# Kernel tuning notes

Hardware: AMD Instinct MI355X
Metric: run time of the kernel (lower is better)

## Reference

```python
import jax, jax.numpy as jnp
import numpy as np
from jax import lax

GROUPS = 32


def _fps(xyz, m):
    # farthest point sampling; indices are non-differentiable selections
    xyz = lax.stop_gradient(xyz)
    B, N, _ = xyz.shape

    def step(carry, _):
        dist, far = carry
        c = jnp.take_along_axis(xyz, far[:, None, None], axis=1)  # [B,1,3]
        d = jnp.sum((xyz - c) ** 2, axis=-1)                       # [B,N]
        dist = jnp.minimum(dist, d)
        return (dist, jnp.argmax(dist, axis=1)), far

    init = (jnp.full((B, N), 1e10, xyz.dtype), jnp.zeros((B,), jnp.int32))
    _, cent = lax.scan(step, init, None, length=m)
    return jnp.transpose(cent)  # [B,m]


def _sqdist(a, b):
    # [B,Na,3] x [B,Nb,3] -> [B,Na,Nb]
    return (jnp.sum(a * a, -1)[:, :, None] + jnp.sum(b * b, -1)[:, None, :]
            - 2.0 * jnp.einsum('bnc,bmc->bnm', a, b))


def _gather(feat, idx):
    # feat [B,S,C], idx [B,N,k] -> [B,N,k,C]
    return jax.vmap(lambda f, i: f[i])(feat, idx)


def _edge_conv(f, idx, W, b):
    nbr = _gather(f, idx)                                # [B,S,k,C]
    ctr = jnp.broadcast_to(f[:, :, None, :], nbr.shape)
    e = jnp.concatenate([ctr, nbr - ctr], axis=-1)       # [B,S,k,2C]
    h = jax.nn.relu(jnp.einsum('bske,ec->bskc', e, W) + b)
    return jnp.max(h, axis=2)                            # [B,S,C']


def _graph_encoder(x, k, layers, Wo, bo):
    d2 = _sqdist(x[..., :3], x[..., :3])
    idx = lax.top_k(-d2, k)[1]                           # kNN on coords (incl. self)
    f = x
    for W, b in layers:
        f = _edge_conv(f, idx, W, b)
    return f @ Wo + bo


def _upsample(fs, xd, xs):
    # 3-NN inverse-distance interpolation, matches torch.cdist/topk path
    d = jnp.sqrt(jnp.maximum(_sqdist(xd, xs), 0.0))      # euclidean like cdist
    negv, idx = lax.top_k(-d, 3)
    w = 1.0 / (-negv + 1e-8)
    w = w / jnp.sum(w, -1, keepdims=True)
    fk = _gather(fs, idx)                                # [B,Nd,3,C]
    return jnp.sum(fk * w[..., None], axis=2)


def _group_norm(x, g, b):
    B, N, C = x.shape
    xg = x.reshape(B, N, GROUPS, C // GROUPS)
    mu = xg.mean(-1, keepdims=True)
    var = xg.var(-1, keepdims=True)
    xn = ((xg - mu) * lax.rsqrt(var + 1e-5)).reshape(B, N, C)
    return xn * g + b


def _pos_encoding(N, d):
    pos = jnp.arange(N, dtype=jnp.float32)[:, None]
    div = jnp.exp(jnp.arange(0, d, 2, dtype=jnp.float32) * (-np.log(10000.0) / d))
    ang = pos * div
    return jnp.stack([jnp.sin(ang), jnp.cos(ang)], axis=-1).reshape(N, d)


def _forward(x,
             e1_W0, e1_b0, e1_W1, e1_b1, e1_Wo, e1_bo,
             e2_W0, e2_b0, e2_W1, e2_b1, e2_Wo, e2_bo,
             e3_W0, e3_b0, e3_W1, e3_b1, e3_W2, e3_b2, e3_Wo, e3_bo,
             f_W1, f_b1, g1_w, g1_b, f_W2, f_b2, g2_w, g2_b):
    B, N, C = x.shape
    encs = [
        (512, 16, [(e1_W0, e1_b0), (e1_W1, e1_b1)], e1_Wo, e1_bo),
        (1024, 32, [(e2_W0, e2_b0), (e2_W1, e2_b1)], e2_Wo, e2_bo),
        (2048, 64, [(e3_W0, e3_b0), (e3_W1, e3_b1), (e3_W2, e3_b2)], e3_Wo, e3_bo),
    ]
    feats = []
    for scale, k, layers, Wo, bo in encs:
        if N > scale:
            idx = _fps(x[..., :3], scale)
            xs = jnp.take_along_axis(x, idx[:, :, None], axis=1)  # [B,scale,C]
        else:
            xs = x
        f = _graph_encoder(xs, k, layers, Wo, bo)
        if f.shape[1] < N:
            f = _upsample(f, x[..., :3], xs[..., :3])
        feats.append(f)
    fused = jnp.concatenate(feats, axis=-1)               # [B,N,1280]
    h = jax.nn.relu(_group_norm(fused @ f_W1 + f_b1, g1_w, g1_b))
    h = jax.nn.relu(_group_norm(h @ f_W2 + f_b2, g2_w, g2_b))
    return h + _pos_encoding(N, h.shape[-1])[None]


def setup_inputs() -> dict:
    key = jax.random.key(0)
    ks = iter(jax.random.split(key, 64))

    def W(shape, s=0.05):
        return jax.random.normal(next(ks), shape, jnp.float32) * s

    inp = {"x": jax.random.normal(next(ks), (2, 4096, 6), jnp.float32)}
    # encoder 1: in 6, hidden [128,256], out 256, k=16
    inp.update(e1_W0=W((12, 128)), e1_b0=jnp.zeros(128), e1_W1=W((256, 256)), e1_b1=jnp.zeros(256),
               e1_Wo=W((256, 256)), e1_bo=jnp.zeros(256))
    # encoder 2: in 6, hidden [256,512], out 512, k=32
    inp.update(e2_W0=W((12, 256)), e2_b0=jnp.zeros(256), e2_W1=W((512, 512)), e2_b1=jnp.zeros(512),
               e2_Wo=W((512, 512)), e2_bo=jnp.zeros(512))
    # encoder 3: in 6, hidden [128,256,512], out 512, k=64
    inp.update(e3_W0=W((12, 128)), e3_b0=jnp.zeros(128), e3_W1=W((256, 256)), e3_b1=jnp.zeros(256),
               e3_W2=W((512, 512)), e3_b2=jnp.zeros(512), e3_Wo=W((512, 512)), e3_bo=jnp.zeros(512))
    # fusion: 1280 -> 512 -> 512 with GroupNorm(32, 512)
    inp.update(f_W1=W((1280, 512)), f_b1=jnp.zeros(512), g1_w=jnp.ones(512), g1_b=jnp.zeros(512),
               f_W2=W((512, 512)), f_b2=jnp.zeros(512), g2_w=jnp.ones(512), g2_b=jnp.zeros(512))
    return inp


def reference(x,
              e1_W0, e1_b0, e1_W1, e1_b1, e1_Wo, e1_bo,
              e2_W0, e2_b0, e2_W1, e2_b1, e2_Wo, e2_bo,
              e3_W0, e3_b0, e3_W1, e3_b1, e3_W2, e3_b2, e3_Wo, e3_bo,
              f_W1, f_b1, g1_w, g1_b, f_W2, f_b2, g2_w, g2_b):
    return _forward(x,
                    e1_W0, e1_b0, e1_W1, e1_b1, e1_Wo, e1_bo,
                    e2_W0, e2_b0, e2_W1, e2_b1, e2_Wo, e2_bo,
                    e3_W0, e3_b0, e3_W1, e3_b1, e3_W2, e3_b2, e3_Wo, e3_bo,
                    f_W1, f_b1, g1_w, g1_b, f_W2, f_b2, g2_w, g2_b)
```

## Files before the change

kernel.cpp:

```cpp
#include <hip/hip_runtime.h>
#include <math.h>

#define OFF_CENT   0x0
#define OFF_XSP    0x20000
#define OFF_XS6    0x40000
#define OFF_KNN    0x60000
#define OFF_F      0x180000
#define OFF_UV     0xA00000
#define OFF_G      0x1A00000
#define OFF_WCAT   0x2200000
#define OFF_BCAT   0x2400000
#define OFF_FUSED  0x2500000
#define OFF_T      0x180000
#define OFF_H1     0x1200000
#define OFF_T2     0x2200000

__device__ __forceinline__ unsigned fkey_flip(float f) {
  unsigned u = __float_as_uint(f);
  return u ^ ((u >> 31) ? 0xFFFFFFFFu : 0x80000000u);
}
__device__ __forceinline__ float fkey_unflip(unsigned k) {
  unsigned u = k ^ ((k >> 31) ? 0x80000000u : 0xFFFFFFFFu);
  return __uint_as_float(u);
}

template<int CTRL>
__device__ __forceinline__ float dpp_max_stepf(float v) {
  int t = __builtin_amdgcn_update_dpp(__float_as_int(v), __float_as_int(v),
                                      CTRL, 0xf, 0xf, false);
  return fmaxf(v, __int_as_float(t));
}
__device__ __forceinline__ float wave64_max(float v) {
  v = dpp_max_stepf<0x111>(v);
  v = dpp_max_stepf<0x112>(v);
  v = dpp_max_stepf<0x114>(v);
  v = dpp_max_stepf<0x118>(v);
  v = dpp_max_stepf<0x142>(v);
  v = dpp_max_stepf<0x143>(v);
  return __int_as_float(__builtin_amdgcn_readlane(__float_as_int(v), 63));
}
__device__ __forceinline__ unsigned long long u64max(unsigned long long a,
                                                    unsigned long long b) {
  return a > b ? a : b;
}

__global__ __launch_bounds__(512) void fps_kernel(const float* __restrict__ x,
                                                  int* __restrict__ cent)
{
  int b = blockIdx.x, tid = threadIdx.x;
  __shared__ float4 C4[4096];
  __shared__ __align__(16) unsigned long long slots[2][8];
  float px[8], py[8], pz[8], dist[8];
#pragma unroll
  for (int i = 0; i < 8; ++i) {
    int p = tid + 512 * i;
    const float* r = x + ((long)b * 4096 + p) * 6;
    px[i] = r[0]; py[i] = r[1]; pz[i] = r[2];
    C4[p] = make_float4(px[i], py[i], pz[i], 0.0f);
    dist[i] = 1e10f;
  }
  if (tid == 0) cent[b * 2048] = 0;
  __syncthreads();
  float4 c0 = C4[0];
  float cx = c0.x, cy = c0.y, cz = c0.z;
  int wid = tid >> 6, lane = tid & 63;
  for (int j = 1; j < 2048; ++j) {
    float m = -1.0f;
#pragma unroll
    for (int i = 0; i < 8; ++i) {
      float dx = __fsub_rn(px[i], cx);
      float dy = __fsub_rn(py[i], cy);
      float dz = __fsub_rn(pz[i], cz);
      float d  = __fadd_rn(__fadd_rn(__fmul_rn(dx,dx), __fmul_rn(dy,dy)), __fmul_rn(dz,dz));
      float nd = fminf(dist[i], d);
      dist[i] = nd;
      m = fmaxf(m, nd);
    }
    float wm = wave64_max(m);
    unsigned long long mm = 0ULL; unsigned ii = 0;
#pragma unroll
    for (int i = 7; i >= 0; --i) {
      unsigned long long mi = __ballot(dist[i] == wm);
      if (mi) { mm = mi; ii = (unsigned)i; }
    }
    int lane_w = __ffsll((unsigned long long)mm) - 1;
    unsigned idx_w = (unsigned)(wid * 64 + lane_w) + 512u * ii;
    if (lane == 0)
      slots[j & 1][wid] = ((unsigned long long)__float_as_uint(wm) << 32)
                        | (unsigned)(0xFFFFFFFFu - idx_w);
    __syncthreads();
    const unsigned long long* sl = slots[j & 1];
    ulonglong2 sA = *(const ulonglong2*)&sl[0];
    ulonglong2 sB = *(const ulonglong2*)&sl[2];
    ulonglong2 sC = *(const ulonglong2*)&sl[4];
    ulonglong2 sD = *(const ulonglong2*)&sl[6];
    unsigned long long kk = u64max(u64max(u64max(sA.x, sA.y), u64max(sB.x, sB.y)),
                                   u64max(u64max(sC.x, sC.y), u64max(sD.x, sD.y)));
    unsigned idx = 0xFFFFFFFFu - (unsigned)kk;
    float4 c = C4[idx];
    cx = c.x; cy = c.y; cz = c.z;
    if (tid == 0) cent[b * 2048 + j] = idx;
  }
}

__global__ void gather_xs_kernel(const float* __restrict__ x, const int* __restrict__ cent,
                                 float* __restrict__ xs6, float4* __restrict__ xsp)
{
  int t = blockIdx.x * 256 + threadIdx.x;
  if (t >= 2 * 2048) return;
  int b = t >> 11;
  int p = cent[t];
  const float* src = x + ((long)b * 4096 + p) * 6;
  float* dst = xs6 + (long)t * 6;
#pragma unroll
  for (int c = 0; c < 6; ++c) dst[c] = src[c];
  xsp[t] = make_float4(src[0], src[1], src[2], 0.0f);
}

template<int S, int K>
__global__ __launch_bounds__(256) void knn_kernel(const float4* __restrict__ xsp,
                                                  int* __restrict__ out)
{
  constexpr int NI = S / 64;
  __shared__ float4 P[S];
  int b = (blockIdx.x * 4) / S;
  int wid = threadIdx.x >> 6, lane = threadIdx.x & 63;
  int s = (blockIdx.x * 4 + wid) & (S - 1);
  for (int i = threadIdx.x; i < S; i += 256) P[i] = xsp[b * 2048 + i];
  __syncthreads();
  float4 Q = P[s];
  float saq = __fadd_rn(__fadd_rn(__fmul_rn(Q.x,Q.x), __fmul_rn(Q.y,Q.y)), __fmul_rn(Q.z,Q.z));
  float dd[NI];
#pragma unroll
  for (int i = 0; i < NI; ++i) {
    float4 c = P[i * 64 + lane];
    float sac = __fadd_rn(__fadd_rn(__fmul_rn(c.x,c.x), __fmul_rn(c.y,c.y)), __fmul_rn(c.z,c.z));
    float dot = __fadd_rn(__fadd_rn(__fmul_rn(Q.x,c.x), __fmul_rn(Q.y,c.y)), __fmul_rn(Q.z,c.z));
    dd[i] = __fsub_rn(__fadd_rn(saq, sac), __fmul_rn(2.0f, dot));
  }
  long obase = ((long)b * S + s) * K;
  for (int t = 0; t < K; ++t) {
    float bv = INFINITY; int bi = 0;
#pragma unroll
    for (int i = 0; i < NI; ++i) if (dd[i] < bv) { bv = dd[i]; bi = i; }
    unsigned long long key = ((unsigned long long)fkey_flip(bv) << 32)
                           | (unsigned)(bi * 64 + lane);
#pragma unroll
    for (int m = 32; m; m >>= 1) {
      unsigned long long o = __shfl_xor(key, m, 64);
      if (o < key) key = o;
    }
    unsigned cand = (unsigned)key;
    if ((int)(cand & 63) == lane) {
      int slot = cand >> 6;
#pragma unroll
      for (int i = 0; i < NI; ++i) if (i == slot) dd[i] = INFINITY;
    }
    if (lane == 0) out[obase + t] = (int)cand;
  }
}

__global__ void wcat_prep(const float* __restrict__ W, const float* __restrict__ bias,
                          int C, int Cp, float* __restrict__ Wcat, float* __restrict__ bcat)
{
  int n2 = 2 * Cp;
  int total = C * n2;
  for (int t = blockIdx.x * 256 + threadIdx.x; t < total + n2; t += gridDim.x * 256) {
    if (t < total) {
      int c = t / n2, n = t % n2;
      Wcat[t] = (n < Cp) ? (W[c * Cp + n] - W[(C + c) * Cp + n]) : W[(C + c) * Cp + (n - Cp)];
    } else {
      int n = t - total;
      bcat[n] = (n < Cp) ? bias[n] : 0.0f;
    }
  }
}

__global__ __launch_bounds__(256) void gemm_bias(
    const float* __restrict__ A, long strideA, int lda,
    const float* __restrict__ W, int N, int K,
    const float* __restrict__ bias,
    float* __restrict__ C, long strideC, int ldc)
{
  A += (long)blockIdx.z * strideA;
  C += (long)blockIdx.z * strideC;
  int rowBase = blockIdx.x * 64, colBase = blockIdx.y * 64;
  __shared__ float As[16][68];
  __shared__ float Ws[16][68];
  int tid = threadIdx.x;
  int tx = tid & 15, ty = tid >> 4;
  float acc[4][4] = {};
  for (int k0 = 0; k0 < K; k0 += 16) {
    {
      int r = tid >> 2, c0 = (tid & 3) * 4;
      const float* Ar = A + (long)(rowBase + r) * lda + k0 + c0;
#pragma unroll
      for (int u = 0; u < 4; ++u) {
        float val = 0.0f;
        if (k0 + c0 + u < K) val = Ar[u];
        As[c0 + u][r] = val;
      }
    }
    {
      int c = tid & 63, kr = tid >> 6;
#pragma unroll
      for (int u = 0; u < 4; ++u) {
        int kk = kr + u * 4;
        float val = 0.0f;
        if (k0 + kk < K) val = W[(long)(k0 + kk) * N + colBase + c];
        Ws[kk][c] = val;
      }
    }
    __syncthreads();
#pragma unroll
    for (int kk = 0; kk < 16; ++kk) {
      float4 av = *(const float4*)&As[kk][ty * 4];
      float4 wv = *(const float4*)&Ws[kk][tx * 4];
      float a_[4] = {av.x, av.y, av.z, av.w};
      float w_[4] = {wv.x, wv.y, wv.z, wv.w};
#pragma unroll
      for (int i = 0; i < 4; ++i)
#pragma unroll
        for (int j = 0; j < 4; ++j)
          acc[i][j] = fmaf(a_[i], w_[j], acc[i][j]);
    }
    __syncthreads();
  }
#pragma unroll
  for (int i = 0; i < 4; ++i) {
    int r = rowBase + ty * 4 + i;
    int c0 = colBase + tx * 4;
    float4 o;
    o.x = acc[i][0] + bias[c0 + 0];
    o.y = acc[i][1] + bias[c0 + 1];
    o.z = acc[i][2] + bias[c0 + 2];
    o.w = acc[i][3] + bias[c0 + 3];
    *(float4*)&C[(long)r * ldc + c0] = o;
  }
}

__global__ __launch_bounds__(256) void gemm_bias_big(
    const float* __restrict__ A, int lda,
    const float* __restrict__ W, int N, int K,
    const float* __restrict__ bias,
    float* __restrict__ C, int ldc)
{
  int rowBase = blockIdx.x * 128, colBase = blockIdx.y * 128;
  __shared__ float As[16][132];
  __shared__ float Ws[16][132];
  int tid = threadIdx.x;
  int tx = tid & 15, ty = tid >> 4;
  float acc[8][8] = {};
  for (int k0 = 0; k0 < K; k0 += 16) {
    {
      int r = tid >> 1, c0 = (tid & 1) * 8;
      const float* Ar = A + (long)(rowBase + r) * lda + k0 + c0;
      float4 v0 = *(const float4*)(Ar);
      float4 v1 = *(const float4*)(Ar + 4);
      As[c0 + 0][r] = v0.x; As[c0 + 1][r] = v0.y; As[c0 + 2][r] = v0.z; As[c0 + 3][r] = v0.w;
      As[c0 + 4][r] = v1.x; As[c0 + 5][r] = v1.y; As[c0 + 6][r] = v1.z; As[c0 + 7][r] = v1.w;
    }
    {
      int kr = tid >> 4, c0 = (tid & 15) * 8;
      const float* Wr = W + (long)(k0 + kr) * N + colBase + c0;
      float4 w0 = *(const float4*)(Wr);
      float4 w1 = *(const float4*)(Wr + 4);
      *(float4*)&Ws[kr][c0]     = w0;
      *(float4*)&Ws[kr][c0 + 4] = w1;
    }
    __syncthreads();
#pragma unroll
    for (int kk = 0; kk < 16; ++kk) {
      float a_[8], w_[8];
      *(float4*)&a_[0] = *(const float4*)&As[kk][ty * 8];
      *(float4*)&a_[4] = *(const float4*)&As[kk][ty * 8 + 4];
      *(float4*)&w_[0] = *(const float4*)&Ws[kk][tx * 8];
      *(float4*)&w_[4] = *(const float4*)&Ws[kk][tx * 8 + 4];
#pragma unroll
      for (int i = 0; i < 8; ++i)
#pragma unroll
        for (int jj = 0; jj < 8; ++jj)
          acc[i][jj] = fmaf(a_[i], w_[jj], acc[i][jj]);
    }
    __syncthreads();
  }
#pragma unroll
  for (int i = 0; i < 8; ++i) {
    int r = rowBase + ty * 8 + i;
    int c0 = colBase + tx * 8;
    float4 o0, o1;
    o0.x = acc[i][0] + bias[c0 + 0];
    o0.y = acc[i][1] + bias[c0 + 1];
    o0.z = acc[i][2] + bias[c0 + 2];
    o0.w = acc[i][3] + bias[c0 + 3];
    o1.x = acc[i][4] + bias[c0 + 4];
    o1.y = acc[i][5] + bias[c0 + 5];
    o1.z = acc[i][6] + bias[c0 + 6];
    o1.w = acc[i][7] + bias[c0 + 7];
    *(float4*)&C[(long)r * ldc + c0]     = o0;
    *(float4*)&C[(long)r * ldc + c0 + 4] = o1;
  }
}

__global__ void edge_agg(const float* __restrict__ UV, const int* __restrict__ idx,
                         int S, int k, int Cp, float* __restrict__ F)
{
  int bs = blockIdx.x;
  int b = bs / S;
  __shared__ int nb[64];
  if ((int)threadIdx.x < k) nb[threadIdx.x] = idx[(long)bs * k + threadIdx.x];
  __syncthreads();
  int ld = 2 * Cp;
  const float* Ub = UV + (long)bs * ld;
  for (int c = threadIdx.x; c < Cp; c += blockDim.x) {
    float m = -INFINITY;
    for (int j = 0; j < k; ++j) {
      float v = UV[(long)(b * S + nb[j]) * ld + Cp + c];
      m = fmaxf(m, v);
    }
    float r = Ub[c] + m;
    F[(long)bs * Cp + c] = r > 0.0f ? r : 0.0f;
  }
}

template<int S, int CP>
__global__ __launch_bounds__(256) void upsample_kernel(
    const float* __restrict__ x, const float4* __restrict__ xsp,
    const float* __restrict__ G, float* __restrict__ fused, int colOff)
{
  constexpr int NI = S / 64;
  __shared__ float4 P[S];
  int b = (blockIdx.x * 4) >> 12;
  int wid = threadIdx.x >> 6, lane = threadIdx.x & 63;
  int n = (blockIdx.x * 4 + wid) & 4095;
  for (int i = threadIdx.x; i < S; i += 256) P[i] = xsp[b * 2048 + i];
  __syncthreads();
  const float* q = x + ((long)b * 4096 + n) * 6;
  float qx = q[0], qy = q[1], qz = q[2];
  float saq = __fadd_rn(__fadd_rn(__fmul_rn(qx,qx), __fmul_rn(qy,qy)), __fmul_rn(qz,qz));
  float dd[NI];
#pragma unroll
  for (int i = 0; i < NI; ++i) {
    float4 c = P[i * 64 + lane];
    float sac = __fadd_rn(__fadd_rn(__fmul_rn(c.x,c.x), __fmul_rn(c.y,c.y)), __fmul_rn(c.z,c.z));
    float dot = __fadd_rn(__fadd_rn(__fmul_rn(qx,c.x), __fmul_rn(qy,c.y)), __fmul_rn(qz,c.z));
    dd[i] = __fsub_rn(__fadd_rn(saq, sac), __fmul_rn(2.0f, dot));
  }
  int id[3]; float w[3];
  for (int t = 0; t < 3; ++t) {
    float bv = INFINITY; int bi = 0;
#pragma unroll
    for (int i = 0; i < NI; ++i) if (dd[i] < bv) { bv = dd[i]; bi = i; }
    unsigned long long key = ((unsigned long long)fkey_flip(bv) << 32)
                           | (unsigned)(bi * 64 + lane);
#pragma unroll
    for (int m = 32; m; m >>= 1) {
      unsigned long long o = __shfl_xor(key, m, 64);
      if (o < key) key = o;
    }
    unsigned cand = (unsigned)key;
    float d2 = fkey_unflip((unsigned)(key >> 32));
    float d = __fsqrt_rn(fmaxf(d2, 0.0f));
    id[t] = (int)cand;
    w[t] = 1.0f / __fadd_rn(d, 1e-8f);
    if ((int)(cand & 63) == lane) {
      int slot = cand >> 6;
#pragma unroll
      for (int i = 0; i < NI; ++i) if (i == slot) dd[i] = INFINITY;
    }
  }
  float wsum = __fadd_rn(__fadd_rn(w[0], w[1]), w[2]);
  float w0 = w[0] / wsum, w1 = w[1] / wsum, w2 = w[2] / wsum;
  const float* g0 = G + (long)(b * S + id[0]) * CP;
  const float* g1 = G + (long)(b * S + id[1]) * CP;
  const float* g2 = G + (long)(b * S + id[2]) * CP;
  float* orow = fused + ((long)b * 4096 + n) * 1280 + colOff;
#pragma unroll
  for (int t = 0; t < CP / 64; ++t) {
    int c = lane + 64 * t;
    float v = __fadd_rn(__fadd_rn(__fmul_rn(w0, g0[c]), __fmul_rn(w1, g1[c])),
                        __fmul_rn(w2, g2[c]));
    orow[c] = v;
  }
}

__global__ __launch_bounds__(256) void gn_kernel(const float* __restrict__ T,
    const float* __restrict__ gw, const float* __restrict__ gb,
    float* __restrict__ out, int addPos)
{
  int t = blockIdx.x * 256 + threadIdx.x;
  int row = t >> 5, g = t & 31;
  const float* p = T + (long)row * 512 + g * 16;
  float v[16];
#pragma unroll
  for (int i = 0; i < 4; ++i) {
    float4 f = *(const float4*)(p + i * 4);
    v[i*4+0] = f.x; v[i*4+1] = f.y; v[i*4+2] = f.z; v[i*4+3] = f.w;
  }
  float s = 0.0f;
#pragma unroll
  for (int i = 0; i < 16; ++i) s += v[i];
  float mu = s * 0.0625f;
  float var = 0.0f;
#pragma unroll
  for (int i = 0; i < 16; ++i) { float d = v[i] - mu; var += d * d; }
  var *= 0.0625f;
  float inv = 1.0f / sqrtf(var + 1e-5f);
  int cbase = g * 16;
  int n = row & 4095;
  float o[16];
#pragma unroll
  for (int i = 0; i < 16; ++i) {
    int c = cbase + i;
    float y = (v[i] - mu) * inv * gw[c] + gb[c];
    y = y > 0.0f ? y : 0.0f;
    if (addPos) {
      int half = c >> 1;
      float div = expf((float)(2 * half) * -0.017988946039016358f);
      float ang = (float)n * div;
      y += (c & 1) ? cosf(ang) : sinf(ang);
    }
    o[i] = y;
  }
  float* d = out + (long)row * 512 + cbase;
#pragma unroll
  for (int i = 0; i < 4; ++i) {
    float4 f; f.x = o[i*4+0]; f.y = o[i*4+1]; f.z = o[i*4+2]; f.w = o[i*4+3];
    *(float4*)(d + i * 4) = f;
  }
}

static inline void launch_gemm(const float* A, long strideA, int lda,
                               const float* W, const float* bias,
                               float* C, long strideC, int ldc,
                               int Mb, int N, int K, int nb, hipStream_t s)
{
  dim3 grid(Mb / 64, N / 64, nb);
  gemm_bias<<<grid, 256, 0, s>>>(A, strideA, lda, W, N, K, bias, C, strideC, ldc);
}
static inline void launch_gemm_big(const float* A, int lda,
                                   const float* W, const float* bias,
                                   float* C, int ldc,
                                   int M, int N, int K, hipStream_t s)
{
  dim3 grid(M / 128, N / 128, 1);
  gemm_bias_big<<<grid, 256, 0, s>>>(A, lda, W, N, K, bias, C, ldc);
}

extern "C" void kernel_launch(void* const* d_in, const int* in_sizes, int n_in,
                              void* d_out, int out_size, void* d_ws, size_t ws_size,
                              hipStream_t stream)
{
  const float* x     = (const float*)d_in[0];
  const float* e1_W0 = (const float*)d_in[1];  const float* e1_b0 = (const float*)d_in[2];
  const float* e1_W1 = (const float*)d_in[3];  const float* e1_b1 = (const float*)d_in[4];
  const float* e1_Wo = (const float*)d_in[5];  const float* e1_bo = (const float*)d_in[6];
  const float* e2_W0 = (const float*)d_in[7];  const float* e2_b0 = (const float*)d_in[8];
  const float* e2_W1 = (const float*)d_in[9];  const float* e2_b1 = (const float*)d_in[10];
  const float* e2_Wo = (const float*)d_in[11]; const float* e2_bo = (const float*)d_in[12];
  const float* e3_W0 = (const float*)d_in[13]; const float* e3_b0 = (const float*)d_in[14];
  const float* e3_W1 = (const float*)d_in[15]; const float* e3_b1 = (const float*)d_in[16];
  const float* e3_W2 = (const float*)d_in[17]; const float* e3_b2 = (const float*)d_in[18];
  const float* e3_Wo = (const float*)d_in[19]; const float* e3_bo = (const float*)d_in[20];
  const float* f_W1  = (const float*)d_in[21]; const float* f_b1  = (const float*)d_in[22];
  const float* g1_w  = (const float*)d_in[23]; const float* g1_b  = (const float*)d_in[24];
  const float* f_W2  = (const float*)d_in[25]; const float* f_b2  = (const float*)d_in[26];
  const float* g2_w  = (const float*)d_in[27]; const float* g2_b  = (const float*)d_in[28];

  char* ws = (char*)d_ws;
  int*    cent  = (int*)(ws + OFF_CENT);
  float4* xsp   = (float4*)(ws + OFF_XSP);
  float*  xs6   = (float*)(ws + OFF_XS6);
  int*    knn   = (int*)(ws + OFF_KNN);
  float*  F     = (float*)(ws + OFF_F);
  float*  UV    = (float*)(ws + OFF_UV);
  float*  G     = (float*)(ws + OFF_G);
  float*  WCAT  = (float*)(ws + OFF_WCAT);
  float*  BCAT  = (float*)(ws + OFF_BCAT);
  float*  FUSED = (float*)(ws + OFF_FUSED);
  float*  T     = (float*)(ws + OFF_T);
  float*  H1    = (float*)(ws + OFF_H1);
  float*  T2    = (float*)(ws + OFF_T2);

  fps_kernel<<<2, 512, 0, stream>>>(x, cent);
  gather_xs_kernel<<<16, 256, 0, stream>>>(x, cent, xs6, xsp);

  knn_kernel<512,16><<<256, 256, 0, stream>>>(xsp, knn);
  wcat_prep<<<256, 256, 0, stream>>>(e1_W0, e1_b0, 6, 128, WCAT, BCAT);
  launch_gemm(xs6, (long)2048*6, 6, WCAT, BCAT, UV, (long)512*256, 256, 512, 256, 6, 2, stream);
  edge_agg<<<dim3(2*512), 128, 0, stream>>>(UV, knn, 512, 16, 128, F);
  wcat_prep<<<256, 256, 0, stream>>>(e1_W1, e1_b1, 128, 256, WCAT, BCAT);
  launch_gemm(F, 0, 128, WCAT, BCAT, UV, 0, 512, 1024, 512, 128, 1, stream);
  edge_agg<<<dim3(2*512), 256, 0, stream>>>(UV, knn, 512, 16, 256, F);
  launch_gemm(F, 0, 256, e1_Wo, e1_bo, G, 0, 256, 1024, 256, 256, 1, stream);
  upsample_kernel<512,256><<<2048, 256, 0, stream>>>(x, xsp, G, FUSED, 0);

  knn_kernel<1024,32><<<512, 256, 0, stream>>>(xsp, knn);
  wcat_prep<<<256, 256, 0, stream>>>(e2_W0, e2_b0, 6, 256, WCAT, BCAT);
  launch_gemm(xs6, (long)2048*6, 6, WCAT, BCAT, UV, (long)1024*512, 512, 1024, 512, 6, 2, stream);
  edge_agg<<<dim3(2*1024), 256, 0, stream>>>(UV, knn, 1024, 32, 256, F);
  wcat_prep<<<256, 256, 0, stream>>>(e2_W1, e2_b1, 256, 512, WCAT, BCAT);
  launch_gemm_big(F, 256, WCAT, BCAT, UV, 1024, 2048, 1024, 256, stream);
  edge_agg<<<dim3(2*1024), 256, 0, stream>>>(UV, knn, 1024, 32, 512, F);
  launch_gemm(F, 0, 512, e2_Wo, e2_bo, G, 0, 512, 2048, 512, 512, 1, stream);
  upsample_kernel<1024,512><<<2048, 256, 0, stream>>>(x, xsp, G, FUSED, 256);

  knn_kernel<2048,64><<<1024, 256, 0, stream>>>(xsp, knn);
  wcat_prep<<<256, 256, 0, stream>>>(e3_W0, e3_b0, 6, 128, WCAT, BCAT);
  launch_gemm(xs6, (long)2048*6, 6, WCAT, BCAT, UV, (long)2048*256, 256, 2048, 256, 6, 2, stream);
  edge_agg<<<dim3(2*2048), 128, 0, stream>>>(UV, knn, 2048, 64, 128, F);
  wcat_prep<<<256, 256, 0, stream>>>(e3_W1, e3_b1, 128, 256, WCAT, BCAT);
  launch_gemm_big(F, 128, WCAT, BCAT, UV, 512, 4096, 512, 128, stream);
  edge_agg<<<dim3(2*2048), 256, 0, stream>>>(UV, knn, 2048, 64, 256, F);
  wcat_prep<<<256, 256, 0, stream>>>(e3_W2, e3_b2, 256, 512, WCAT, BCAT);
  launch_gemm_big(F, 256, WCAT, BCAT, UV, 1024, 4096, 1024, 256, stream);
  edge_agg<<<dim3(2*2048), 256, 0, stream>>>(UV, knn, 2048, 64, 512, F);
  launch_gemm_big(F, 512, e3_Wo, e3_bo, G, 512, 4096, 512, 512, stream);
  upsample_kernel<2048,512><<<2048, 256, 0, stream>>>(x, xsp, G, FUSED, 768);

  launch_gemm_big(FUSED, 1280, f_W1, f_b1, T, 512, 8192, 512, 1280, stream);
  gn_kernel<<<1024, 256, 0, stream>>>(T, g1_w, g1_b, H1, 0);
  launch_gemm_big(H1, 512, f_W2, f_b2, T2, 512, 8192, 512, 512, stream);
  gn_kernel<<<1024, 256, 0, stream>>>(T2, g2_w, g2_b, (float*)d_out, 1);
}
```

Measured before the change: 2.309 ms.

## Use split-bf16 MFMA GEMM and vectorize edge aggregation and upsample gathers

Replaces the FP32 SIMT 128x128 GEMM with a matrix-core kernel that splits each fp32 operand into high and low bf16 parts and issues three MFMA 16x16x32 products, keeping near-fp32 accuracy. Several medium GEMMs previously on the 64-tile path now use it as well. Edge aggregation and the upsample gather are rewritten to use float4 loads and stores, with the edge thread count tied to channel width. The GEMM loads W with strided scalar reads, writes scalar outputs and has no double buffering, and the bf16x3 scheme loses a little precision compared with fp32.

```diff
diff --git a/kernel.cpp b/kernel.cpp
--- a/kernel.cpp
+++ b/kernel.cpp
@@ -239,67 +239,109 @@
   }
 }
 
-__global__ __launch_bounds__(256) void gemm_bias_big(
+typedef __attribute__((ext_vector_type(8))) short bf16x8;
+typedef __attribute__((ext_vector_type(4))) float f32x4;
+
+__device__ __forceinline__ unsigned short f2bf_rn(float f) {
+  unsigned u = __float_as_uint(f);
+  unsigned r = u + 0x7FFFu + ((u >> 16) & 1u);
+  return (unsigned short)(r >> 16);
+}
+__device__ __forceinline__ float bf2f(unsigned short h) {
+  return __uint_as_float(((unsigned)h) << 16);
+}
+__device__ __forceinline__ void cvt4(const float4 v, int2& hi, int2& lo) {
+  unsigned short h0 = f2bf_rn(v.x), h1 = f2bf_rn(v.y);
+  unsigned short h2 = f2bf_rn(v.z), h3 = f2bf_rn(v.w);
+  unsigned short l0 = f2bf_rn(v.x - bf2f(h0)), l1 = f2bf_rn(v.y - bf2f(h1));
+  unsigned short l2 = f2bf_rn(v.z - bf2f(h2)), l3 = f2bf_rn(v.w - bf2f(h3));
+  hi.x = (int)((unsigned)h0 | ((unsigned)h1 << 16));
+  hi.y = (int)((unsigned)h2 | ((unsigned)h3 << 16));
+  lo.x = (int)((unsigned)l0 | ((unsigned)l1 << 16));
+  lo.y = (int)((unsigned)l2 | ((unsigned)l3 << 16));
+}
+
+__global__ __launch_bounds__(256) void gemm_mfma(
     const float* __restrict__ A, int lda,
     const float* __restrict__ W, int N, int K,
     const float* __restrict__ bias,
     float* __restrict__ C, int ldc)
 {
+  __shared__ unsigned short Ah[128][40], Al[128][40];
+  __shared__ unsigned short Bh[128][40], Bl[128][40];
+  int tid = threadIdx.x;
+  int lane = tid & 63, wv = tid >> 6;
+  int wr = wv >> 1, wc = wv & 1;
+  int l15 = lane & 15, l16 = lane >> 4;
   int rowBase = blockIdx.x * 128, colBase = blockIdx.y * 128;
-  __shared__ float As[16][132];
-  __shared__ float Ws[16][132];
-  int tid = threadIdx.x;
-  int tx = tid & 15, ty = tid >> 4;
-  float acc[8][8] = {};
-  for (int k0 = 0; k0 < K; k0 += 16) {
+  f32x4 acc[4][4];
+#pragma unroll
+  for (int mb = 0; mb < 4; ++mb)
+#pragma unroll
+    for (int nb = 0; nb < 4; ++nb) acc[mb][nb] = 0.0f;
+
+  int r_st = tid >> 1, h_st = tid & 1;
+  for (int k0 = 0; k0 < K; k0 += 32) {
     {
-      int r = tid >> 1, c0 = (tid & 1) * 8;
-      const float* Ar = A + (long)(rowBase + r) * lda + k0 + c0;
-      float4 v0 = *(const float4*)(Ar);
-      float4 v1 = *(const float4*)(Ar + 4);
-      As[c0 + 0][r] = v0.x; As[c0 + 1][r] = v0.y; As[c0 + 2][r] = v0.z; As[c0 + 3][r] = v0.w;
-      As[c0 + 4][r] = v1.x; As[c0 + 5][r] = v1.y; As[c0 + 6][r] = v1.z; As[c0 + 7][r] = v1.w;
+      const float* Ap = A + (long)(rowBase + r_st) * lda + k0 + h_st * 16;
+#pragma unroll
+      for (int e = 0; e < 16; e += 4) {
+        float4 v = *(const float4*)(Ap + e);
+        int2 hi, lo; cvt4(v, hi, lo);
+        *(int2*)&Ah[r_st][h_st * 16 + e] = hi;
+        *(int2*)&Al[r_st][h_st * 16 + e] = lo;
+      }
     }
     {
-      int kr = tid >> 4, c0 = (tid & 15) * 8;
-      const float* Wr = W + (long)(k0 + kr) * N + colBase + c0;
-      float4 w0 = *(const float4*)(Wr);
-      float4 w1 = *(const float4*)(Wr + 4);
-      *(float4*)&Ws[kr][c0]     = w0;
-      *(float4*)&Ws[kr][c0 + 4] = w1;
+      const float* Wp = W + (long)(k0 + h_st * 16) * N + colBase + r_st;
+#pragma unroll
+      for (int e = 0; e < 16; e += 4) {
+        float4 v;
+        v.x = Wp[(long)(e + 0) * N];
+        v.y = Wp[(long)(e + 1) * N];
+        v.z = Wp[(long)(e + 2) * N];
+        v.w = Wp[(long)(e + 3) * N];
+        int2 hi, lo; cvt4(v, hi, lo);
+        *(int2*)&Bh[r_st][h_st * 16 + e] = hi;
+        *(int2*)&Bl[r_st][h_st * 16 + e] = lo;
+      }
     }
     __syncthreads();
-#pragma unroll
-    for (int kk = 0; kk < 16; ++kk) {
-      float a_[8], w_[8];
-      *(float4*)&a_[0] = *(const float4*)&As[kk][ty * 8];
-      *(float4*)&a_[4] = *(const float4*)&As[kk][ty * 8 + 4];
-      *(float4*)&w_[0] = *(const float4*)&Ws[kk][tx * 8];
-      *(float4*)&w_[4] = *(const float4*)&Ws[kk][tx * 8 + 4];
-#pragma unroll
-      for (int i = 0; i < 8; ++i)
-#pragma unroll
-        for (int jj = 0; jj < 8; ++jj)
-          acc[i][jj] = fmaf(a_[i], w_[jj], acc[i][jj]);
-    }
+    bf16x8 ah[4], al[4], bh[4], bl[4];
+#pragma unroll
+    for (int mb = 0; mb < 4; ++mb) {
+      int r = wr * 64 + mb * 16 + l15;
+      ah[mb] = *(const bf16x8*)&Ah[r][l16 * 8];
+      al[mb] = *(const bf16x8*)&Al[r][l16 * 8];
+    }
+#pragma unroll
+    for (int nb = 0; nb < 4; ++nb) {
+      int c = wc * 64 + nb * 16 + l15;
+      bh[nb] = *(const bf16x8*)&Bh[c][l16 * 8];
+      bl[nb] = *(const bf16x8*)&Bl[c][l16 * 8];
+    }
+#pragma unroll
+    for (int mb = 0; mb < 4; ++mb)
+#pragma unroll
+      for (int nb = 0; nb < 4; ++nb) {
+        acc[mb][nb] = __builtin_amdgcn_mfma_f32_16x16x32_bf16(ah[mb], bh[nb], acc[mb][nb], 0, 0, 0);
+        acc[mb][nb] = __builtin_amdgcn_mfma_f32_16x16x32_bf16(al[mb], bh[nb], acc[mb][nb], 0, 0, 0);
+        acc[mb][nb] = __builtin_amdgcn_mfma_f32_16x16x32_bf16(ah[mb], bl[nb], acc[mb][nb], 0, 0, 0);
+      }
     __syncthreads();
   }
 #pragma unroll
-  for (int i = 0; i < 8; ++i) {
-    int r = rowBase + ty * 8 + i;
-    int c0 = colBase + tx * 8;
-    float4 o0, o1;
-    o0.x = acc[i][0] + bias[c0 + 0];
-    o0.y = acc[i][1] + bias[c0 + 1];
-    o0.z = acc[i][2] + bias[c0 + 2];
-    o0.w = acc[i][3] + bias[c0 + 3];
-    o1.x = acc[i][4] + bias[c0 + 4];
-    o1.y = acc[i][5] + bias[c0 + 5];
-    o1.z = acc[i][6] + bias[c0 + 6];
-    o1.w = acc[i][7] + bias[c0 + 7];
-    *(float4*)&C[(long)r * ldc + c0]     = o0;
-    *(float4*)&C[(long)r * ldc + c0 + 4] = o1;
-  }
+  for (int mb = 0; mb < 4; ++mb)
+#pragma unroll
+    for (int nb = 0; nb < 4; ++nb) {
+      int c = colBase + wc * 64 + nb * 16 + l15;
+      float bs = bias[c];
+#pragma unroll
+      for (int r = 0; r < 4; ++r) {
+        int row = rowBase + wr * 64 + mb * 16 + l16 * 4 + r;
+        C[(long)row * ldc + c] = acc[mb][nb][r] + bs;
+      }
+    }
 }
 
 __global__ void edge_agg(const float* __restrict__ UV, const int* __restrict__ idx,
@@ -311,15 +353,23 @@
   if ((int)threadIdx.x < k) nb[threadIdx.x] = idx[(long)bs * k + threadIdx.x];
   __syncthreads();
   int ld = 2 * Cp;
-  const float* Ub = UV + (long)bs * ld;
-  for (int c = threadIdx.x; c < Cp; c += blockDim.x) {
-    float m = -INFINITY;
+  int nf4 = Cp >> 2;
+  for (int c4 = threadIdx.x; c4 < nf4; c4 += blockDim.x) {
+    float4 m = make_float4(-INFINITY, -INFINITY, -INFINITY, -INFINITY);
     for (int j = 0; j < k; ++j) {
-      float v = UV[(long)(b * S + nb[j]) * ld + Cp + c];
-      m = fmaxf(m, v);
-    }
-    float r = Ub[c] + m;
-    F[(long)bs * Cp + c] = r > 0.0f ? r : 0.0f;
+      const float4* vp = (const float4*)(UV + (long)(b * S + nb[j]) * ld + Cp);
+      float4 v = vp[c4];
+      m.x = fmaxf(m.x, v.x); m.y = fmaxf(m.y, v.y);
+      m.z = fmaxf(m.z, v.z); m.w = fmaxf(m.w, v.w);
+    }
+    float4 u = ((const float4*)(UV + (long)bs * ld))[c4];
+    float4 o;
+    o.x = u.x + m.x; o.y = u.y + m.y; o.z = u.z + m.z; o.w = u.w + m.w;
+    o.x = o.x > 0.0f ? o.x : 0.0f;
+    o.y = o.y > 0.0f ? o.y : 0.0f;
+    o.z = o.z > 0.0f ? o.z : 0.0f;
+    o.w = o.w > 0.0f ? o.w : 0.0f;
+    ((float4*)(F + (long)bs * Cp))[c4] = o;
   }
 }
 
@@ -371,16 +421,20 @@
   }
   float wsum = __fadd_rn(__fadd_rn(w[0], w[1]), w[2]);
   float w0 = w[0] / wsum, w1 = w[1] / wsum, w2 = w[2] / wsum;
-  const float* g0 = G + (long)(b * S + id[0]) * CP;
-  const float* g1 = G + (long)(b * S + id[1]) * CP;
-  const float* g2 = G + (long)(b * S + id[2]) * CP;
-  float* orow = fused + ((long)b * 4096 + n) * 1280 + colOff;
-#pragma unroll
-  for (int t = 0; t < CP / 64; ++t) {
-    int c = lane + 64 * t;
-    float v = __fadd_rn(__fadd_rn(__fmul_rn(w0, g0[c]), __fmul_rn(w1, g1[c])),
-                        __fmul_rn(w2, g2[c]));
-    orow[c] = v;
+  const float4* g0 = (const float4*)(G + (long)(b * S + id[0]) * CP);
+  const float4* g1 = (const float4*)(G + (long)(b * S + id[1]) * CP);
+  const float4* g2 = (const float4*)(G + (long)(b * S + id[2]) * CP);
+  float4* orow = (float4*)(fused + ((long)b * 4096 + n) * 1280 + colOff);
+#pragma unroll
+  for (int t = 0; t < CP / 256; ++t) {
+    int c4 = lane + 64 * t;
+    float4 a = g0[c4], bb4 = g1[c4], cc = g2[c4];
+    float4 v;
+    v.x = __fadd_rn(__fadd_rn(__fmul_rn(w0, a.x), __fmul_rn(w1, bb4.x)), __fmul_rn(w2, cc.x));
+    v.y = __fadd_rn(__fadd_rn(__fmul_rn(w0, a.y), __fmul_rn(w1, bb4.y)), __fmul_rn(w2, cc.y));
+    v.z = __fadd_rn(__fadd_rn(__fmul_rn(w0, a.z), __fmul_rn(w1, bb4.z)), __fmul_rn(w2, cc.z));
+    v.w = __fadd_rn(__fadd_rn(__fmul_rn(w0, a.w), __fmul_rn(w1, bb4.w)), __fmul_rn(w2, cc.w));
+    orow[c4] = v;
   }
 }
 
@@ -438,13 +492,19 @@
   dim3 grid(Mb / 64, N / 64, nb);
   gemm_bias<<<grid, 256, 0, s>>>(A, strideA, lda, W, N, K, bias, C, strideC, ldc);
 }
-static inline void launch_gemm_big(const float* A, int lda,
-                                   const float* W, const float* bias,
-                                   float* C, int ldc,
-                                   int M, int N, int K, hipStream_t s)
+static inline void launch_mfma(const float* A, int lda,
+                               const float* W, const float* bias,
+                               float* C, int ldc,
+                               int M, int N, int K, hipStream_t s)
 {
   dim3 grid(M / 128, N / 128, 1);
-  gemm_bias_big<<<grid, 256, 0, s>>>(A, lda, W, N, K, bias, C, ldc);
+  gemm_mfma<<<grid, 256, 0, s>>>(A, lda, W, N, K, bias, C, ldc);
+}
+static inline void launch_edge(const float* UV, const int* knn, int S, int k, int Cp,
+                               float* F, hipStream_t s)
+{
+  int threads = Cp / 4 < 64 ? 64 : Cp / 4;
+  edge_agg<<<dim3(2 * S), threads, 0, s>>>(UV, knn, S, k, Cp, F);
 }
 
 extern "C" void kernel_launch(void* const* d_in, const int* in_sizes, int n_in,
@@ -488,38 +548,38 @@
   knn_kernel<512,16><<<256, 256, 0, stream>>>(xsp, knn);
   wcat_prep<<<256, 256, 0, stream>>>(e1_W0, e1_b0, 6, 128, WCAT, BCAT);
   launch_gemm(xs6, (long)2048*6, 6, WCAT, BCAT, UV, (long)512*256, 256, 512, 256, 6, 2, stream);
-  edge_agg<<<dim3(2*512), 128, 0, stream>>>(UV, knn, 512, 16, 128, F);
+  launch_edge(UV, knn, 512, 16, 128, F, stream);
   wcat_prep<<<256, 256, 0, stream>>>(e1_W1, e1_b1, 128, 256, WCAT, BCAT);
-  launch_gemm(F, 0, 128, WCAT, BCAT, UV, 0, 512, 1024, 512, 128, 1, stream);
-  edge_agg<<<dim3(2*512), 256, 0, stream>>>(UV, knn, 512, 16, 256, F);
-  launch_gemm(F, 0, 256, e1_Wo, e1_bo, G, 0, 256, 1024, 256, 256, 1, stream);
+  launch_mfma(F, 128, WCAT, BCAT, UV, 512, 1024, 512, 128, stream);
+  launch_edge(UV, knn, 512, 16, 256, F, stream);
+  launch_mfma(F, 256, e1_Wo, e1_bo, G, 256, 1024, 256, 256, stream);
   upsample_kernel<512,256><<<2048, 256, 0, stream>>>(x, xsp, G, FUSED, 0);
 
   knn_kernel<1024,32><<<512, 256, 0, stream>>>(xsp, knn);
   wcat_prep<<<256, 256, 0, stream>>>(e2_W0, e2_b0, 6, 256, WCAT, BCAT);
   launch_gemm(xs6, (long)2048*6, 6, WCAT, BCAT, UV, (long)1024*512, 512, 1024, 512, 6, 2, stream);
-  edge_agg<<<dim3(2*1024), 256, 0, stream>>>(UV, knn, 1024, 32, 256, F);
+  launch_edge(UV, knn, 1024, 32, 256, F, stream);
   wcat_prep<<<256, 256, 0, stream>>>(e2_W1, e2_b1, 256, 512, WCAT, BCAT);
-  launch_gemm_big(F, 256, WCAT, BCAT, UV, 1024, 2048, 1024, 256, stream);
-  edge_agg<<<dim3(2*1024), 256, 0, stream>>>(UV, knn, 1024, 32, 512, F);
-  launch_gemm(F, 0, 512, e2_Wo, e2_bo, G, 0, 512, 2048, 512, 512, 1, stream);
+  launch_mfma(F, 256, WCAT, BCAT, UV, 1024, 2048, 1024, 256, stream);
+  launch_edge(UV, knn, 1024, 32, 512, F, stream);
+  launch_mfma(F, 512, e2_Wo, e2_bo, G, 512, 2048, 512, 512, stream);
   upsample_kernel<1024,512><<<2048, 256, 0, stream>>>(x, xsp, G, FUSED, 256);
 
   knn_kernel<2048,64><<<1024, 256, 0, stream>>>(xsp, knn);
   wcat_prep<<<256, 256, 0, stream>>>(e3_W0, e3_b0, 6, 128, WCAT, BCAT);
   launch_gemm(xs6, (long)2048*6, 6, WCAT, BCAT, UV, (long)2048*256, 256, 2048, 256, 6, 2, stream);
-  edge_agg<<<dim3(2*2048), 128, 0, stream>>>(UV, knn, 2048, 64, 128, F);
+  launch_edge(UV, knn, 2048, 64, 128, F, stream);
   wcat_prep<<<256, 256, 0, stream>>>(e3_W1, e3_b1, 128, 256, WCAT, BCAT);
-  launch_gemm_big(F, 128, WCAT, BCAT, UV, 512, 4096, 512, 128, stream);
-  edge_agg<<<dim3(2*2048), 256, 0, stream>>>(UV, knn, 2048, 64, 256, F);
+  launch_mfma(F, 128, WCAT, BCAT, UV, 512, 4096, 512, 128, stream);
+  launch_edge(UV, knn, 2048, 64, 256, F, stream);
   wcat_prep<<<256, 256, 0, stream>>>(e3_W2, e3_b2, 256, 512, WCAT, BCAT);
-  launch_gemm_big(F, 256, WCAT, BCAT, UV, 1024, 4096, 1024, 256, stream);
-  edge_agg<<<dim3(2*2048), 256, 0, stream>>>(UV, knn, 2048, 64, 512, F);
-  launch_gemm_big(F, 512, e3_Wo, e3_bo, G, 512, 4096, 512, 512, stream);
+  launch_mfma(F, 256, WCAT, BCAT, UV, 1024, 4096, 1024, 256, stream);
+  launch_edge(UV, knn, 2048, 64, 512, F, stream);
+  launch_mfma(F, 512, e3_Wo, e3_bo, G, 512, 4096, 512, 512, stream);
   upsample_kernel<2048,512><<<2048, 256, 0, stream>>>(x, xsp, G, FUSED, 768);
 
-  launch_gemm_big(FUSED, 1280, f_W1, f_b1, T, 512, 8192, 512, 1280, stream);
+  launch_mfma(FUSED, 1280, f_W1, f_b1, T, 512, 8192, 512, 1280, stream);
   gn_kernel<<<1024, 256, 0, stream>>>(T, g1_w, g1_b, H1, 0);
-  launch_gemm_big(H1, 512, f_W2, f_b2, T2, 512, 8192, 512, 512, stream);
+  launch_mfma(H1, 512, f_W2, f_b2, T2, 512, 8192, 512, 512, stream);
   gn_kernel<<<1024, 256, 0, stream>>>(T2, g2_w, g2_b, (float*)d_out, 1);
 }
```

Result: faster. 1.863 ms, median of 2 (-19.3%).
